# Optimization experiments

Measured on AMD Instinct MI355X. Metric: run time of the kernel, lower is better.

Reference implementation:

```python
import jax, jax.numpy as jnp
import numpy as np

# ---- static sizes ----
B, N, F_IN = 256, 512, 128          # graphs, nodes-per-graph, node feature dim
LATENT = [128, 128, 128, 128]        # per-layer GNN widths (conv_params)
D = sum(LATENT)                      # dense_dim = 512
OUT = 128                            # output_dim
DEG = 16                             # avg degree -> edges per node
TN = B * N                           # 131072 total nodes
E = TN * DEG                         # 2097152 directed edges


def setup_inputs() -> dict:
    key = jax.random.key(0)
    ks = jax.random.split(key, 10)
    node_feat = jax.random.normal(ks[0], (TN, F_IN), dtype=jnp.float32)
    # edges are intra-graph: global node id = graph_base + local id in [0, N)
    base = jnp.repeat(jnp.arange(B, dtype=jnp.int32) * N, N * DEG)  # [E]
    edge_src = base + jax.random.randint(ks[1], (E,), 0, N, dtype=jnp.int32)
    edge_dst = base + jax.random.randint(ks[2], (E,), 0, N, dtype=jnp.int32)
    conv_W = jax.random.normal(ks[3], (len(LATENT), 128, 128), dtype=jnp.float32) * 0.08
    conv_b = jnp.zeros((len(LATENT), 128), dtype=jnp.float32)
    att_W = jax.random.normal(ks[4], (D, D), dtype=jnp.float32) * 0.04
    att_b = jnp.zeros((D,), dtype=jnp.float32)
    att_v = jax.random.normal(ks[5], (D,), dtype=jnp.float32) * 0.06
    out_W = jax.random.normal(ks[6], (D, OUT), dtype=jnp.float32) * 0.06
    out_b = jnp.zeros((OUT,), dtype=jnp.float32)
    return {"node_feat": node_feat, "edge_src": edge_src, "edge_dst": edge_dst,
            "conv_W": conv_W, "conv_b": conv_b, "att_W": att_W, "att_b": att_b,
            "att_v": att_v, "out_W": out_W, "out_b": out_b}


def reference(node_feat, edge_src, edge_dst, conv_W, conv_b, att_W, att_b, att_v, out_W, out_b):
    # node_degs = degree + 1 (n2n row sums + 1), matching graph.degs + 1
    ones = jnp.ones((E,), dtype=node_feat.dtype)
    degs = jax.ops.segment_sum(ones, edge_dst, num_segments=TN) + 1.0   # [TN]
    degs = degs[:, None]

    # graph convolution layers: spmm(A, h) + h -> Linear -> /deg -> tanh
    h = node_feat
    layers = []
    for l in range(len(LATENT)):
        agg = jax.ops.segment_sum(h[edge_src], edge_dst, num_segments=TN) + h  # [TN, d]
        lin = agg @ conv_W[l] + conv_b[l]
        h = jnp.tanh(lin / degs)
        layers.append(h)
    cat = jnp.concatenate(layers, axis=1)        # [TN, D]

    # per-graph additive attention pooling (FlexAddAttention aggregation)
    x = cat.reshape(B, N, D)                     # uniform graph sizes
    scores = jnp.einsum('bnd,d->bn', jnp.tanh(x @ att_W + att_b), att_v)  # [B, N]
    attn = jax.nn.softmax(scores, axis=1)
    pooled = jnp.einsum('bn,bnd->bd', attn, x)   # [B, D]

    # out_params + relu (second relu in original is idempotent)
    return jax.nn.relu(pooled @ out_W + out_b)   # [B, OUT]
```

## Files before the change

kernel.cpp:

```cpp
#include <hip/hip_runtime.h>
#include <hip/hip_bf16.h>

#define TN 131072
#define NB 256
#define NN 512
#define FD 128
#define DD 512
#define NE 2097152
#define NEB 8192
#define NL 4
#define PITCH 136
#define CHK 32
#define NCH 16
#define CICAP 832

typedef __attribute__((ext_vector_type(8))) short bf16x8;
typedef __attribute__((ext_vector_type(4))) float f32x4;

__device__ __forceinline__ float b2f(unsigned int u) {
    union { unsigned int i; float f; } c; c.i = u << 16; return c.f;
}
__device__ __forceinline__ unsigned short f2b(float f) {
    union { float f; unsigned int i; } c; c.f = f;
    unsigned int x = c.i;
    return (unsigned short)((x + 0x7fffu + ((x >> 16) & 1u)) >> 16);
}
__device__ __forceinline__ void add2(float& a0, float& a1, unsigned int v) {
    union { unsigned int u; float f; } lo, hi;
    lo.u = v << 16; hi.u = v & 0xffff0000u;
    a0 += lo.f; a1 += hi.f;
}
__device__ __forceinline__ void set2(float& a0, float& a1, unsigned int v) {
    union { unsigned int u; float f; } lo, hi;
    lo.u = v << 16; hi.u = v & 0xffff0000u;
    a0 = lo.f; a1 = hi.f;
}
__device__ __forceinline__ uint4 packv8(const float* a) {
    uint4 p;
    p.x = (unsigned int)f2b(a[0]) | ((unsigned int)f2b(a[1]) << 16);
    p.y = (unsigned int)f2b(a[2]) | ((unsigned int)f2b(a[3]) << 16);
    p.z = (unsigned int)f2b(a[4]) | ((unsigned int)f2b(a[5]) << 16);
    p.w = (unsigned int)f2b(a[6]) | ((unsigned int)f2b(a[7]) << 16);
    return p;
}
__device__ __forceinline__ float ftanh(float x) {
    float xc = fminf(fmaxf(x, -9.0f), 9.0f);
    float e = __expf(2.0f * xc);
    return (e - 1.0f) * __builtin_amdgcn_rcpf(e + 1.0f);
}
__device__ __forceinline__ void gl_lds16(const unsigned short* g, unsigned short* l) {
    __builtin_amdgcn_global_load_lds(
        (const __attribute__((address_space(1))) unsigned int*)g,
        (__attribute__((address_space(3))) unsigned int*)l,
        16, 0, 0);
}
__device__ __forceinline__ void dot2acc(float& acc, unsigned int p, unsigned int ones) {
    asm("v_dot2_f32_bf16 %0, %1, %2, %0" : "+v"(acc) : "v"(p), "v"(ones));
}

__global__ __launch_bounds__(1024) void csr_b_k(
    const int* __restrict__ src, const int* __restrict__ dst,
    int* __restrict__ row_ptr, int* __restrict__ col_off,
    float* __restrict__ degs)
{
    __shared__ int cnt[NN];
    __shared__ int ss[NN];
    int b = blockIdx.x, t = threadIdx.x;
    int e0 = b * NEB;
    if (t < NN) cnt[t] = 0;
    __syncthreads();
    #pragma unroll
    for (int i = 0; i < NEB / 1024; i++) {
        int d = dst[e0 + t + i * 1024] & (NN - 1);
        atomicAdd(&cnt[d], 1);
    }
    __syncthreads();
    int c = 0;
    if (t < NN) { c = cnt[t]; ss[t] = c; }
    __syncthreads();
    for (int off = 1; off < NN; off <<= 1) {
        int v = (t < NN && t >= off) ? ss[t - off] : 0;
        __syncthreads();
        if (t < NN) ss[t] += v;
        __syncthreads();
    }
    if (t < NN) {
        int excl = ss[t] - c;
        int gid = b * NN + t;
        row_ptr[gid] = e0 + excl;
        degs[gid] = (float)(c + 1);
        cnt[t] = excl;
        if (b == NB - 1 && t == NN - 1) row_ptr[TN] = NE;
    }
    __syncthreads();
    #pragma unroll
    for (int i = 0; i < NEB / 1024; i++) {
        int e = e0 + t + i * 1024;
        int d = dst[e] & (NN - 1);
        int p = atomicAdd(&cnt[d], 1);
        col_off[e0 + p] = (src[e] & (NN - 1)) * (PITCH * 2);
    }
}

__global__ __launch_bounds__(256) void transpose_cast_k(const float* __restrict__ W,
                                                        unsigned short* __restrict__ Wt) {
    __shared__ float tile[32][33];
    int k0 = blockIdx.x * 32, n0 = blockIdx.y * 32;
    int tx = threadIdx.x & 31, ty = threadIdx.x >> 5;
    #pragma unroll
    for (int i = 0; i < 32; i += 8)
        tile[ty + i][tx] = W[(size_t)(k0 + ty + i) * DD + n0 + tx];
    __syncthreads();
    #pragma unroll
    for (int i = 0; i < 32; i += 8)
        Wt[(size_t)(n0 + ty + i) * DD + k0 + tx] = f2b(tile[tx][ty + i]);
}

__global__ __launch_bounds__(256) void transp_convW_k(const float* __restrict__ W,
                                                      unsigned short* __restrict__ Wt) {
    __shared__ float tile[32][33];
    const float* Wl = W + (size_t)blockIdx.z * FD * FD;
    unsigned short* Wtl = Wt + (size_t)blockIdx.z * FD * FD;
    int f0 = blockIdx.x * 32, o0 = blockIdx.y * 32;
    int tx = threadIdx.x & 31, ty = threadIdx.x >> 5;
    #pragma unroll
    for (int i = 0; i < 32; i += 8)
        tile[ty + i][tx] = Wl[(size_t)(f0 + ty + i) * FD + o0 + tx];
    __syncthreads();
    #pragma unroll
    for (int i = 0; i < 32; i += 8)
        Wtl[(size_t)(o0 + ty + i) * FD + f0 + tx] = f2b(tile[tx][ty + i]);
}

__global__ __launch_bounds__(1024) void conv_all_k(
    const float* __restrict__ node_feat,
    const unsigned short* __restrict__ Wt,
    const float* __restrict__ bias,
    const int* __restrict__ rp, const int* __restrict__ coff,
    const float* __restrict__ degs,
    unsigned short* __restrict__ cat)
{
    __shared__ unsigned short hW[NN * PITCH];
    __shared__ unsigned short agg[2][CHK * PITCH];
    __shared__ int ciL[2][CICAP];
    const int tid = threadIdx.x;
    const int g0 = blockIdx.x * NN;
    const int lane = tid & 63, w = tid >> 6;
    const int lr = lane & 15, lh = lane >> 4;
    const int mo = w >> 1, nd = w & 1;
    const int gn = tid >> 5;
    const int gs = tid & 31;
    const char* hWb = (const char*)hW;
    const unsigned int SEL0 = 0x01000504u;
    const unsigned int SEL1 = 0x03020706u;
    const unsigned int ONES = 0x3F803F80u;

    #pragma unroll
    for (int i = 0; i < 8; i++) {
        int u = tid + i * 1024;
        int row = u >> 4, cu = u & 15;
        const float4* s4 = (const float4*)(node_feat + (size_t)(g0 + row) * FD + cu * 8);
        float4 x = s4[0], y = s4[1];
        float tmp[8] = {x.x, x.y, x.z, x.w, y.x, y.y, y.z, y.w};
        *(uint4*)&hW[row * PITCH + cu * 8] = packv8(tmp);
    }
    __syncthreads();

    auto do_gather = [&](int nl, int rs, int re, int eb, const int* cib,
                         unsigned short* buf) {
        const char* rowb = hWb + nl * (PITCH * 2);
        uint2 v = *(const uint2*)(rowb + gs * 8);
        float a0, a1, a2, a3;
        set2(a0, a1, v.x); set2(a2, a3, v.y);
        int r1 = re;
        int rlim = eb + CICAP; if (r1 > rlim) r1 = rlim;
        int j = rs;
        for (; j + 8 <= r1; j += 8) {
            int off[8];
            #pragma unroll
            for (int i = 0; i < 8; i++) off[i] = cib[j - eb + i];
            uint2 u[8];
            #pragma unroll
            for (int i = 0; i < 8; i++) u[i] = *(const uint2*)(hWb + off[i] + gs * 8);
            #pragma unroll
            for (int i = 0; i < 4; i++) {
                unsigned int x1 = u[2 * i].x, x2 = u[2 * i + 1].x;
                unsigned int y1 = u[2 * i].y, y2 = u[2 * i + 1].y;
                dot2acc(a0, __builtin_amdgcn_perm(x1, x2, SEL0), ONES);
                dot2acc(a1, __builtin_amdgcn_perm(x1, x2, SEL1), ONES);
                dot2acc(a2, __builtin_amdgcn_perm(y1, y2, SEL0), ONES);
                dot2acc(a3, __builtin_amdgcn_perm(y1, y2, SEL1), ONES);
            }
        }
        for (; j + 2 <= r1; j += 2) {
            int o0 = cib[j - eb], o1 = cib[j - eb + 1];
            uint2 u0 = *(const uint2*)(hWb + o0 + gs * 8);
            uint2 u1 = *(const uint2*)(hWb + o1 + gs * 8);
            dot2acc(a0, __builtin_amdgcn_perm(u0.x, u1.x, SEL0), ONES);
            dot2acc(a1, __builtin_amdgcn_perm(u0.x, u1.x, SEL1), ONES);
            dot2acc(a2, __builtin_amdgcn_perm(u0.y, u1.y, SEL0), ONES);
            dot2acc(a3, __builtin_amdgcn_perm(u0.y, u1.y, SEL1), ONES);
        }
        if (j < r1) {
            int off = cib[j - eb];
            uint2 u = *(const uint2*)(hWb + off + gs * 8);
            add2(a0, a1, u.x); add2(a2, a3, u.y);
            j = r1;
        }
        for (; j < re; j++) {
            int off = coff[j];
            uint2 u = *(const uint2*)(hWb + off + gs * 8);
            add2(a0, a1, u.x); add2(a2, a3, u.y);
        }
        uint2 pk;
        pk.x = (unsigned int)f2b(a0) | ((unsigned int)f2b(a1) << 16);
        pk.y = (unsigned int)f2b(a2) | ((unsigned int)f2b(a3) << 16);
        *(uint2*)&buf[gn * PITCH + gs * 4] = pk;
    };

    for (int l = 0; l < NL; l++) {
        bf16x8 af[4];
        #pragma unroll
        for (int ks = 0; ks < 4; ks++)
            af[ks] = *(const bf16x8*)&Wt[((size_t)l * FD + mo * 16 + lr) * FD + ks * 32 + lh * 8];
        float4 bs = *(const float4*)&bias[l * FD + mo * 16 + lh * 4];

        {
            int eb0 = rp[g0];
            int cnt0 = rp[g0 + CHK] - eb0;      if (cnt0 > CICAP) cnt0 = CICAP;
            int eb1 = rp[g0 + CHK];
            int cnt1 = rp[g0 + 2 * CHK] - eb1;  if (cnt1 > CICAP) cnt1 = CICAP;
            int rs0 = rp[g0 + gn], re0 = rp[g0 + gn + 1];
            if (tid < cnt0) ciL[0][tid] = coff[eb0 + tid];
            if (tid < cnt1) ciL[1][tid] = coff[eb1 + tid];
            __syncthreads();
            do_gather(gn, rs0, re0, eb0, ciL[0], agg[0]);
        }
        __syncthreads();

        for (int c = 0; c < NCH; c++) {
            int cur = c & 1;
            int rs_n = 0, re_n = 0, eb_n = 0;
            if (c < NCH - 1) {
                eb_n = rp[g0 + (c + 1) * CHK];
                rs_n = rp[g0 + (c + 1) * CHK + gn];
                re_n = rp[g0 + (c + 1) * CHK + gn + 1];
            }
            int scnt = 0, sval = 0;
            if (c <= NCH - 3) {
                int eb2 = rp[g0 + (c + 2) * CHK];
                scnt = rp[g0 + (c + 3) * CHK] - eb2; if (scnt > CICAP) scnt = CICAP;
                if (tid < scnt) sval = coff[eb2 + tid];
            }
            f32x4 cc = (f32x4){0.f, 0.f, 0.f, 0.f};
            {
                const unsigned short* ab = &agg[cur][(nd * 16 + lr) * PITCH + lh * 8];
                #pragma unroll
                for (int ks = 0; ks < 4; ks++) {
                    bf16x8 bfv = *(const bf16x8*)&ab[ks * 32];
                    cc = __builtin_amdgcn_mfma_f32_16x16x32_bf16(af[ks], bfv, cc, 0, 0, 0);
                }
            }
            {
                int dstl = c * CHK + nd * 16 + lr;
                float rd = __builtin_amdgcn_rcpf(degs[g0 + dstl]);
                float t0 = ftanh((cc[0] + bs.x) * rd);
                float t1 = ftanh((cc[1] + bs.y) * rd);
                float t2 = ftanh((cc[2] + bs.z) * rd);
                float t3 = ftanh((cc[3] + bs.w) * rd);
                uint2 pk;
                pk.x = (unsigned int)f2b(t0) | ((unsigned int)f2b(t1) << 16);
                pk.y = (unsigned int)f2b(t2) | ((unsigned int)f2b(t3) << 16);
                *(uint2*)&cat[(size_t)(g0 + dstl) * DD + l * FD + mo * 16 + lh * 4] = pk;
            }
            if (tid < scnt) ciL[cur][tid] = sval;
            if (c < NCH - 1)
                do_gather((c + 1) * CHK + gn, rs_n, re_n, eb_n, ciL[(c + 1) & 1], agg[cur ^ 1]);
            __syncthreads();
        }

        if (l < NL - 1) {
            #pragma unroll
            for (int i = 0; i < 8; i++) {
                int u = tid + i * 1024;
                int row = u >> 4, cu = u & 15;
                uint4 v = *(const uint4*)&cat[(size_t)(g0 + row) * DD + l * FD + cu * 8];
                *(uint4*)&hW[row * PITCH + cu * 8] = v;
            }
            __syncthreads();
        }
    }
}

__global__ __launch_bounds__(256) void scores_k(
    const unsigned short* __restrict__ X,
    const unsigned short* __restrict__ Wt,
    const float* __restrict__ bv, const float* __restrict__ vv,
    float* __restrict__ sp)
{
    __shared__ unsigned short sXl[128 * 64];
    __shared__ unsigned short sWl[128 * 64];
    int bid = blockIdx.x;
    int swz = (bid & 7) * 512 + (bid >> 3);
    int bx = swz >> 2, by = swz & 3;
    int tid = threadIdx.x;
    int lane = tid & 63, wid = tid >> 6;
    int wm = wid >> 1, wn = wid & 1;
    int m0 = bx * 128;
    int n0 = by * 128;
    int lr = lane & 15, lh = lane >> 4;

    f32x4 acc[4][4];
    #pragma unroll
    for (int mi = 0; mi < 4; mi++)
        #pragma unroll
        for (int ni = 0; ni < 4; ni++)
            acc[mi][ni] = (f32x4){0.f, 0.f, 0.f, 0.f};

    for (int k0 = 0; k0 < DD; k0 += 64) {
        __syncthreads();
        #pragma unroll
        for (int i = 0; i < 4; i++) {
            int u = (i << 8) + tid;
            int row = u >> 3, cu = u & 7;
            int su = cu ^ (row & 7);
            gl_lds16(&X[(size_t)(m0 + row) * DD + k0 + su * 8], &sXl[u * 8]);
            gl_lds16(&Wt[(size_t)(n0 + row) * DD + k0 + su * 8], &sWl[u * 8]);
        }
        __syncthreads();
        #pragma unroll
        for (int kk = 0; kk < 64; kk += 32) {
            int cu0 = (kk >> 3) + lh;
            bf16x8 afv[4], bfv[4];
            #pragma unroll
            for (int mi = 0; mi < 4; mi++) {
                int rr = wm * 64 + mi * 16 + lr;
                afv[mi] = *(const bf16x8*)&sXl[rr * 64 + ((cu0 ^ (rr & 7)) << 3)];
            }
            #pragma unroll
            for (int ni = 0; ni < 4; ni++) {
                int rr = wn * 64 + ni * 16 + lr;
                bfv[ni] = *(const bf16x8*)&sWl[rr * 64 + ((cu0 ^ (rr & 7)) << 3)];
            }
            #pragma unroll
            for (int mi = 0; mi < 4; mi++)
                #pragma unroll
                for (int ni = 0; ni < 4; ni++)
                    acc[mi][ni] = __builtin_amdgcn_mfma_f32_16x16x32_bf16(
                        afv[mi], bfv[ni], acc[mi][ni], 0, 0, 0);
        }
    }

    float vcol[4], bcol[4];
    #pragma unroll
    for (int ni = 0; ni < 4; ni++) {
        int col = n0 + wn * 64 + ni * 16 + lr;
        vcol[ni] = vv[col];
        bcol[ni] = bv[col];
    }
    #pragma unroll
    for (int mi = 0; mi < 4; mi++) {
        #pragma unroll
        for (int r = 0; r < 4; r++) {
            float part = 0.f;
            #pragma unroll
            for (int ni = 0; ni < 4; ni++)
                part += ftanh(acc[mi][ni][r] + bcol[ni]) * vcol[ni];
            part += __shfl_xor(part, 1);
            part += __shfl_xor(part, 2);
            part += __shfl_xor(part, 4);
            part += __shfl_xor(part, 8);
            if (lr == 0) {
                int row = m0 + wm * 64 + mi * 16 + lh * 4 + r;
                sp[(size_t)row * 8 + by * 2 + wn] = part;
            }
        }
    }
}

__global__ __launch_bounds__(512) void pool_k(
    const float* __restrict__ sp, const unsigned short* __restrict__ X,
    float* __restrict__ pooled)
{
    __shared__ float sattn[512];
    __shared__ float wmax[8];
    __shared__ float wsum[8];
    __shared__ float pred[3][512];
    int b = blockIdx.x, t = threadIdx.x;
    int lane = t & 63, wid = t >> 6;

    float s;
    {
        const float4* p = (const float4*)&sp[((size_t)b * NN + t) * 8];
        float4 x = p[0], y = p[1];
        s = x.x + x.y + x.z + x.w + y.x + y.y + y.z + y.w;
    }
    float m = s;
    #pragma unroll
    for (int off = 1; off < 64; off <<= 1) m = fmaxf(m, __shfl_xor(m, off));
    if (lane == 0) wmax[wid] = m;
    __syncthreads();
    m = wmax[0];
    #pragma unroll
    for (int i = 1; i < 8; i++) m = fmaxf(m, wmax[i]);
    float e = expf(s - m);
    float ssum = e;
    #pragma unroll
    for (int off = 1; off < 64; off <<= 1) ssum += __shfl_xor(ssum, off);
    if (lane == 0) wsum[wid] = ssum;
    __syncthreads();
    float tot = wsum[0];
    #pragma unroll
    for (int i = 1; i < 8; i++) tot += wsum[i];
    sattn[t] = e * (1.0f / tot);
    __syncthreads();

    int rg = t >> 7, tc = t & 127;
    float4 acc = {0.f, 0.f, 0.f, 0.f};
    const unsigned short* Xb = X + (size_t)b * NN * DD;
    int n0 = rg * 128;
    #pragma unroll 4
    for (int n = n0; n < n0 + 128; n++) {
        float a = sattn[n];
        uint2 px = *(const uint2*)&Xb[(size_t)n * DD + tc * 4];
        acc.x += a * b2f(px.x & 0xffff);
        acc.y += a * b2f(px.x >> 16);
        acc.z += a * b2f(px.y & 0xffff);
        acc.w += a * b2f(px.y >> 16);
    }
    if (rg > 0) *(float4*)&pred[rg - 1][tc * 4] = acc;
    __syncthreads();
    if (rg == 0) {
        #pragma unroll
        for (int g = 0; g < 3; g++) {
            float4 q = *(const float4*)&pred[g][tc * 4];
            acc.x += q.x; acc.y += q.y; acc.z += q.z; acc.w += q.w;
        }
        *(float4*)&pooled[b * DD + tc * 4] = acc;
    }
}

__global__ void out_k(const float* __restrict__ pooled, const float* __restrict__ Wo,
                      const float* __restrict__ bo, float* __restrict__ out) {
    int b = blockIdx.x, c = threadIdx.x;
    float acc = 0.f;
    const float* p = pooled + b * DD;
    for (int k = 0; k < DD; k++) acc += p[k] * Wo[k * 128 + c];
    out[b * 128 + c] = fmaxf(acc + bo[c], 0.f);
}

extern "C" void kernel_launch(void* const* d_in, const int* in_sizes, int n_in,
                              void* d_out, int out_size, void* d_ws, size_t ws_size,
                              hipStream_t stream)
{
    const float* node_feat = (const float*)d_in[0];
    const int*   edge_src  = (const int*)d_in[1];
    const int*   edge_dst  = (const int*)d_in[2];
    const float* conv_W    = (const float*)d_in[3];
    const float* conv_b    = (const float*)d_in[4];
    const float* att_W     = (const float*)d_in[5];
    const float* att_b     = (const float*)d_in[6];
    const float* att_v     = (const float*)d_in[7];
    const float* out_W     = (const float*)d_in[8];
    const float* out_b     = (const float*)d_in[9];
    float* out = (float*)d_out;
    (void)in_sizes; (void)n_in; (void)out_size;

    char* ws = (char*)d_ws;
    size_t off = 0;
    auto alloc = [&](size_t bytes) {
        void* p = ws + off;
        off += (bytes + 255) & ~(size_t)255;
        return p;
    };
    unsigned short* cat   = (unsigned short*)alloc((size_t)TN * DD * 2);
    int*   row_ptr = (int*)alloc((size_t)(TN + 1) * 4);
    int*   col_off = (int*)alloc((size_t)NE * 4);
    float* degs    = (float*)alloc((size_t)TN * 4);
    float* sp      = (float*)alloc((size_t)TN * 8 * 4);
    unsigned short* attWt = (unsigned short*)alloc((size_t)DD * DD * 2);
    unsigned short* convWt = (unsigned short*)alloc((size_t)NL * FD * FD * 2);
    float* pooled  = (float*)alloc((size_t)NB * DD * 4);
    if (off > ws_size) return;

    csr_b_k<<<NB, 1024, 0, stream>>>(edge_src, edge_dst, row_ptr, col_off, degs);
    transpose_cast_k<<<dim3(DD / 32, DD / 32), 256, 0, stream>>>(att_W, attWt);
    transp_convW_k<<<dim3(FD / 32, FD / 32, NL), 256, 0, stream>>>(conv_W, convWt);

    conv_all_k<<<NB, 1024, 0, stream>>>(node_feat, convWt, conv_b,
                                        row_ptr, col_off, degs, cat);

    scores_k<<<4096, 256, 0, stream>>>(cat, attWt, att_b, att_v, sp);
    pool_k<<<NB, 512, 0, stream>>>(sp, cat, pooled);
    out_k<<<NB, 128, 0, stream>>>(pooled, out_W, out_b, out);
}
```

Measured before the change: 359.2 us.

## Keep full X row-block resident in LDS and sweep all attention columns per block

The scores kernel now loads a 128x512 bf16 tile of the concatenated features into LDS once per block and loops over all 512 output columns in two 256-wide passes, streaming only chunks of the transposed attention weight. This removes the fourfold re-reading of X from global memory across column tiles and halves the partial-score buffer. The cost is a large LDS footprint of about 160 KB per block, which limits occupancy, and fewer blocks (1024) with more serialized work per block.

New measurement: 359.6 us. Within noise of the previous version (+0.1%).

```diff
diff --git a/kernel.cpp b/kernel.cpp
--- a/kernel.cpp
+++ b/kernel.cpp
@@ -292,87 +292,111 @@
     }
 }
 
-__global__ __launch_bounds__(256) void scores_k(
+__global__ __launch_bounds__(512) void scores_k(
     const unsigned short* __restrict__ X,
     const unsigned short* __restrict__ Wt,
     const float* __restrict__ bv, const float* __restrict__ vv,
     float* __restrict__ sp)
 {
-    __shared__ unsigned short sXl[128 * 64];
-    __shared__ unsigned short sWl[128 * 64];
+    __shared__ unsigned short sXl[128 * 512];
+    __shared__ unsigned short sWc[256 * 64];
     int bid = blockIdx.x;
-    int swz = (bid & 7) * 512 + (bid >> 3);
-    int bx = swz >> 2, by = swz & 3;
+    int swz = (bid & 7) * 128 + (bid >> 3);
+    int m0 = swz * 128;
     int tid = threadIdx.x;
-    int lane = tid & 63, wid = tid >> 6;
-    int wm = wid >> 1, wn = wid & 1;
-    int m0 = bx * 128;
-    int n0 = by * 128;
+    int lane = tid & 63, w = tid >> 6;
+    int wm = w >> 2, wn = w & 3;
     int lr = lane & 15, lh = lane >> 4;
 
-    f32x4 acc[4][4];
+    #pragma unroll
+    for (int i = 0; i < 16; i++) {
+        int u = tid + i * 512;
+        int row = u >> 6, ul = u & 63;
+        int su = ul ^ (row & 7);
+        gl_lds16(&X[(size_t)(m0 + row) * DD + su * 8], &sXl[u * 8]);
+    }
+
+    float part[4][4];
     #pragma unroll
     for (int mi = 0; mi < 4; mi++)
         #pragma unroll
-        for (int ni = 0; ni < 4; ni++)
-            acc[mi][ni] = (f32x4){0.f, 0.f, 0.f, 0.f};
-
-    for (int k0 = 0; k0 < DD; k0 += 64) {
-        __syncthreads();
-        #pragma unroll
-        for (int i = 0; i < 4; i++) {
-            int u = (i << 8) + tid;
-            int row = u >> 3, cu = u & 7;
-            int su = cu ^ (row & 7);
-            gl_lds16(&X[(size_t)(m0 + row) * DD + k0 + su * 8], &sXl[u * 8]);
-            gl_lds16(&Wt[(size_t)(n0 + row) * DD + k0 + su * 8], &sWl[u * 8]);
-        }
-        __syncthreads();
-        #pragma unroll
-        for (int kk = 0; kk < 64; kk += 32) {
-            int cu0 = (kk >> 3) + lh;
-            bf16x8 afv[4], bfv[4];
-            #pragma unroll
-            for (int mi = 0; mi < 4; mi++) {
-                int rr = wm * 64 + mi * 16 + lr;
-                afv[mi] = *(const bf16x8*)&sXl[rr * 64 + ((cu0 ^ (rr & 7)) << 3)];
-            }
-            #pragma unroll
-            for (int ni = 0; ni < 4; ni++) {
-                int rr = wn * 64 + ni * 16 + lr;
-                bfv[ni] = *(const bf16x8*)&sWl[rr * 64 + ((cu0 ^ (rr & 7)) << 3)];
-            }
-            #pragma unroll
-            for (int mi = 0; mi < 4; mi++)
+        for (int r = 0; r < 4; r++) part[mi][r] = 0.f;
+
+    #pragma unroll
+    for (int p = 0; p < 2; p++) {
+        int n0 = p * 256;
+        f32x4 acc[4][4];
+        #pragma unroll
+        for (int mi = 0; mi < 4; mi++)
+            #pragma unroll
+            for (int ni = 0; ni < 4; ni++)
+                acc[mi][ni] = (f32x4){0.f, 0.f, 0.f, 0.f};
+
+        for (int kc = 0; kc < 8; kc++) {
+            __syncthreads();
+            #pragma unroll
+            for (int i = 0; i < 4; i++) {
+                int u = tid + i * 512;
+                int row = u >> 3, ul = u & 7;
+                int su = ul ^ (row & 7);
+                gl_lds16(&Wt[(size_t)(n0 + row) * DD + kc * 64 + su * 8], &sWc[u * 8]);
+            }
+            __syncthreads();
+            #pragma unroll
+            for (int kk = 0; kk < 2; kk++) {
+                bf16x8 afv[4], bfv[4];
+                #pragma unroll
+                for (int mi = 0; mi < 4; mi++) {
+                    int rr = wm * 64 + mi * 16 + lr;
+                    int ulog = kc * 8 + kk * 4 + lh;
+                    afv[mi] = *(const bf16x8*)&sXl[rr * 512 + ((ulog ^ (rr & 7)) << 3)];
+                }
+                #pragma unroll
+                for (int ni = 0; ni < 4; ni++) {
+                    int rn = wn * 64 + ni * 16 + lr;
+                    int ulog = kk * 4 + lh;
+                    bfv[ni] = *(const bf16x8*)&sWc[rn * 64 + ((ulog ^ (rn & 7)) << 3)];
+                }
+                #pragma unroll
+                for (int mi = 0; mi < 4; mi++)
+                    #pragma unroll
+                    for (int ni = 0; ni < 4; ni++)
+                        acc[mi][ni] = __builtin_amdgcn_mfma_f32_16x16x32_bf16(
+                            afv[mi], bfv[ni], acc[mi][ni], 0, 0, 0);
+            }
+        }
+
+        float vcol[4], bcol[4];
+        #pragma unroll
+        for (int ni = 0; ni < 4; ni++) {
+            int col = n0 + wn * 64 + ni * 16 + lr;
+            vcol[ni] = vv[col];
+            bcol[ni] = bv[col];
+        }
+        #pragma unroll
+        for (int mi = 0; mi < 4; mi++)
+            #pragma unroll
+            for (int r = 0; r < 4; r++) {
+                float s = 0.f;
                 #pragma unroll
                 for (int ni = 0; ni < 4; ni++)
-                    acc[mi][ni] = __builtin_amdgcn_mfma_f32_16x16x32_bf16(
-                        afv[mi], bfv[ni], acc[mi][ni], 0, 0, 0);
-        }
-    }
-
-    float vcol[4], bcol[4];
-    #pragma unroll
-    for (int ni = 0; ni < 4; ni++) {
-        int col = n0 + wn * 64 + ni * 16 + lr;
-        vcol[ni] = vv[col];
-        bcol[ni] = bv[col];
-    }
+                    s += ftanh(acc[mi][ni][r] + bcol[ni]) * vcol[ni];
+                part[mi][r] += s;
+            }
+    }
+
     #pragma unroll
     for (int mi = 0; mi < 4; mi++) {
         #pragma unroll
         for (int r = 0; r < 4; r++) {
-            float part = 0.f;
-            #pragma unroll
-            for (int ni = 0; ni < 4; ni++)
-                part += ftanh(acc[mi][ni][r] + bcol[ni]) * vcol[ni];
-            part += __shfl_xor(part, 1);
-            part += __shfl_xor(part, 2);
-            part += __shfl_xor(part, 4);
-            part += __shfl_xor(part, 8);
+            float s = part[mi][r];
+            s += __shfl_xor(s, 1);
+            s += __shfl_xor(s, 2);
+            s += __shfl_xor(s, 4);
+            s += __shfl_xor(s, 8);
             if (lr == 0) {
                 int row = m0 + wm * 64 + mi * 16 + lh * 4 + r;
-                sp[(size_t)row * 8 + by * 2 + wn] = part;
+                sp[(size_t)row * 4 + wn] = s;
             }
         }
     }
@@ -391,9 +415,8 @@
 
     float s;
     {
-        const float4* p = (const float4*)&sp[((size_t)b * NN + t) * 8];
-        float4 x = p[0], y = p[1];
-        s = x.x + x.y + x.z + x.w + y.x + y.y + y.z + y.w;
+        float4 x = *(const float4*)&sp[((size_t)b * NN + t) * 4];
+        s = x.x + x.y + x.z + x.w;
     }
     float m = s;
     #pragma unroll
@@ -477,7 +500,7 @@
     int*   row_ptr = (int*)alloc((size_t)(TN + 1) * 4);
     int*   col_off = (int*)alloc((size_t)NE * 4);
     float* degs    = (float*)alloc((size_t)TN * 4);
-    float* sp      = (float*)alloc((size_t)TN * 8 * 4);
+    float* sp      = (float*)alloc((size_t)TN * 4 * 4);
     unsigned short* attWt = (unsigned short*)alloc((size_t)DD * DD * 2);
     unsigned short* convWt = (unsigned short*)alloc((size_t)NL * FD * FD * 2);
     float* pooled  = (float*)alloc((size_t)NB * DD * 4);
@@ -490,7 +513,7 @@
     conv_all_k<<<NB, 1024, 0, stream>>>(node_feat, convWt, conv_b,
                                         row_ptr, col_off, degs, cat);
 
-    scores_k<<<4096, 256, 0, stream>>>(cat, attWt, att_b, att_v, sp);
+    scores_k<<<1024, 512, 0, stream>>>(cat, attWt, att_b, att_v, sp);
     pool_k<<<NB, 512, 0, stream>>>(sp, cat, pooled);
     out_k<<<NB, 128, 0, stream>>>(pooled, out_W, out_b, out);
 }
```
